# Performance work log

Hardware: AMD Instinct MI355X
Metric: run time of the kernel (lower is better)

## Reference

```python
import jax, jax.numpy as jnp
import numpy as np

DIM = 100            # lattice side length
N = DIM * DIM        # data_dim = dim ** lattice_dim
BATCH = 512
INIT_SIGMA = 0.15
INIT_BIAS = 0.0


def lattice_adjacency(dim):
    """Adjacency of a circular (periodic) 2D lattice, matching ig.Graph.Lattice(dim=[dim,dim], circular=True)."""
    idx = np.arange(dim * dim).reshape(dim, dim)
    A = np.zeros((dim * dim, dim * dim), dtype=np.float32)
    for sh in ((1, 0), (-1, 0), (0, 1), (0, -1)):
        nb = np.roll(idx, sh, axis=(0, 1))
        A[idx.ravel(), nb.ravel()] = 1.0
    return A


def setup_inputs() -> dict:
    key = jax.random.key(0)
    kx, = jax.random.split(key, 1)
    # binary spin configurations in {0,1}, as sampled by the model's Bernoulli init_dist
    x = jax.random.bernoulli(kx, 0.5, (BATCH, N)).astype(jnp.float32)
    G = jnp.asarray(lattice_adjacency(DIM))          # [N, N] lattice adjacency
    sigma = jnp.asarray(INIT_SIGMA, dtype=jnp.float32)  # scalar coupling
    bias = jnp.full((N,), INIT_BIAS, dtype=jnp.float32)  # [N]
    return {"x": x, "G": G, "sigma": sigma, "bias": bias}


def reference(x, G, sigma, bias):
    # flatten any trailing dims: x -> [B, N]
    x = x.reshape(x.shape[0], -1)
    x = 2.0 * x - 1.0                 # {0,1} -> {-1,+1} spins
    J = G * sigma                     # [N, N]
    xg = x @ J                        # [B, N] dense GEMM (the kernel target)
    xgx = jnp.sum(xg * x, axis=-1)    # quadratic form x^T J x, [B]
    b = x @ bias                      # [B]
    return xgx + b
```

## Files before the change

### kernel.cpp

```cpp
#include <hip/hip_runtime.h>


constexpr int DIM = 100;
constexpr int N   = DIM * DIM;
constexpr int NG  = N / 4;
constexpr int GPR = DIM / 4;

__global__ __launch_bounds__(1024)
void lattice_ising_kernel(const float* __restrict__ x,
                          const float* __restrict__ sigma_p,
                          const float* __restrict__ bias,
                          float* __restrict__ out)
{
    __shared__ float s[N];
    __shared__ float red[16];

    const int b   = blockIdx.x;
    const int tid = threadIdx.x;
    const float* __restrict__ xr = x + (size_t)b * N;
    float4* s4 = reinterpret_cast<float4*>(s);

    for (int i = tid; i < NG; i += 1024) {
        float4 v = reinterpret_cast<const float4*>(xr)[i];
        v.x = 2.0f * v.x - 1.0f;
        v.y = 2.0f * v.y - 1.0f;
        v.z = 2.0f * v.z - 1.0f;
        v.w = 2.0f * v.w - 1.0f;
        s4[i] = v;
    }
    __syncthreads();

    float acc_hv = 0.0f, acc_b = 0.0f;
    for (int g = tid; g < NG; g += 1024) {
        const float4 v = s4[g];

        int gd = g + GPR;
        if (gd >= NG) gd -= NG;
        const float4 w = s4[gd];

        const int c  = g - GPR * (g / GPR);
        const int gr = (c == GPR - 1) ? g - (GPR - 1) : g + 1;
        const float rightx = s[4 * gr];

        acc_hv += v.x * v.y + v.y * v.z + v.z * v.w + v.w * rightx
                + v.x * w.x + v.y * w.y + v.z * w.z + v.w * w.w;

        const float4 bv = reinterpret_cast<const float4*>(bias)[g];
        acc_b += v.x * bv.x + v.y * bv.y + v.z * bv.z + v.w * bv.w;
    }

    const float sigma = sigma_p[0];
    float acc = fmaf(2.0f * sigma, acc_hv, acc_b);

    #pragma unroll
    for (int off = 32; off > 0; off >>= 1)
        acc += __shfl_down(acc, off, 64);

    const int wid = tid >> 6;
    if ((tid & 63) == 0) red[wid] = acc;
    __syncthreads();
    if (tid == 0) {
        float t = 0.0f;
        #pragma unroll
        for (int i = 0; i < 16; ++i) t += red[i];
        out[b] = t;
    }
}

extern "C" void kernel_launch(void* const* d_in, const int* in_sizes, int n_in,
                              void* d_out, int out_size, void* d_ws, size_t ws_size,
                              hipStream_t stream)
{
    const float* x     = (const float*)d_in[0];
    const float* sigma = (const float*)d_in[2];
    const float* bias  = (const float*)d_in[3];
    float* out = (float*)d_out;

    const int B = out_size;
    lattice_ising_kernel<<<B, 1024, 0, stream>>>(x, sigma, bias, out);
}
```

Baseline: 9.407 us.

## Drop shared-memory staging by expanding spin products algebraically over raw inputs

Removes the shared-memory copy of the transformed spins and the barrier that follows it, and reads the {0,1} inputs directly from global memory. The quadratic and bias terms are rewritten in terms of raw x by expanding (2x-1) products, which needs extra accumulators for sum(x) and sum(bias) plus a constant 4*sigma*N term. Neighbour values are now re-read from global memory (three loads per group), which relies on cache hits, and the expanded form may change floating-point rounding slightly.

```diff
diff --git a/kernel.cpp b/kernel.cpp
--- a/kernel.cpp
+++ b/kernel.cpp
@@ -12,45 +12,43 @@
                           const float* __restrict__ bias,
                           float* __restrict__ out)
 {
-    __shared__ float s[N];
     __shared__ float red[16];
 
     const int b   = blockIdx.x;
     const int tid = threadIdx.x;
-    const float* __restrict__ xr = x + (size_t)b * N;
-    float4* s4 = reinterpret_cast<float4*>(s);
+    const float4* __restrict__ x4 = reinterpret_cast<const float4*>(x + (size_t)b * N);
+    const float*  __restrict__ xr = reinterpret_cast<const float*>(x4);
+    const float4* __restrict__ b4 = reinterpret_cast<const float4*>(bias);
 
-    for (int i = tid; i < NG; i += 1024) {
-        float4 v = reinterpret_cast<const float4*>(xr)[i];
-        v.x = 2.0f * v.x - 1.0f;
-        v.y = 2.0f * v.y - 1.0f;
-        v.z = 2.0f * v.z - 1.0f;
-        v.w = 2.0f * v.w - 1.0f;
-        s4[i] = v;
-    }
-    __syncthreads();
+    float accP = 0.0f;
+    float accX = 0.0f;
+    float accXB = 0.0f;
+    float accBT = 0.0f;
 
-    float acc_hv = 0.0f, acc_b = 0.0f;
     for (int g = tid; g < NG; g += 1024) {
-        const float4 v = s4[g];
+        const float4 v = x4[g];
 
         int gd = g + GPR;
         if (gd >= NG) gd -= NG;
-        const float4 w = s4[gd];
+        const float4 w = x4[gd];
 
         const int c  = g - GPR * (g / GPR);
         const int gr = (c == GPR - 1) ? g - (GPR - 1) : g + 1;
-        const float rightx = s[4 * gr];
+        const float rightx = xr[4 * gr];
 
-        acc_hv += v.x * v.y + v.y * v.z + v.z * v.w + v.w * rightx
-                + v.x * w.x + v.y * w.y + v.z * w.z + v.w * w.w;
+        accP += v.x * v.y + v.y * v.z + v.z * v.w + v.w * rightx
+              + v.x * w.x + v.y * w.y + v.z * w.z + v.w * w.w;
+        accX += (v.x + v.y) + (v.z + v.w);
 
-        const float4 bv = reinterpret_cast<const float4*>(bias)[g];
-        acc_b += v.x * bv.x + v.y * bv.y + v.z * bv.z + v.w * bv.w;
+        const float4 bv = b4[g];
+        accXB += v.x * bv.x + v.y * bv.y + v.z * bv.z + v.w * bv.w;
+        accBT += (bv.x + bv.y) + (bv.z + bv.w);
     }
 
     const float sigma = sigma_p[0];
-    float acc = fmaf(2.0f * sigma, acc_hv, acc_b);
+    float acc = fmaf(8.0f * sigma, accP,
+                fmaf(-16.0f * sigma, accX,
+                fmaf(2.0f, accXB, -accBT)));
 
     #pragma unroll
     for (int off = 32; off > 0; off >>= 1)
@@ -60,7 +58,7 @@
     if ((tid & 63) == 0) red[wid] = acc;
     __syncthreads();
     if (tid == 0) {
-        float t = 0.0f;
+        float t = 4.0f * sigma * (float)N;
         #pragma unroll
         for (int i = 0; i < 16; ++i) t += red[i];
         out[b] = t;
```

New measurement: 10.16 us. 8.0% more time.
